# Optimization experiments

Measured on AMD Instinct MI355X. Metric: run time of the kernel, lower is better.

The kernel has to match this reference:

```python
import jax, jax.numpy as jnp
import numpy as np

N, S, HIDDEN, K, B = 20000, 16, 128, 64, 256
EPS = 0.1      # entropic blur / regularization used both in Sinkhorn and in log_pi
ITERS = 20     # fixed-point iterations (geomloss runs to tolerance; 20 converges here)


def setup_inputs() -> dict:
    key = jax.random.key(0)
    k1, k2, k3 = jax.random.split(key, 3)
    limit = float(np.sqrt(6.0 / (K + HIDDEN)))  # xavier_uniform for codebook
    return {
        "node_distributions": jax.random.normal(k1, (N, S, HIDDEN), jnp.float32),
        "batch_idx": jax.random.randint(k2, (N,), 0, B),
        "codebook": jax.random.uniform(k3, (K, HIDDEN), jnp.float32, -limit, limit),
        "log_codebook_prior": jnp.zeros((K,), jnp.float32),
        "num_graphs": B,
    }


def _sq_cost(x, y):
    # x [N,S,d], y [K,d] -> [N,S,K] squared euclidean = cdist(p=2)**2
    x2 = jnp.sum(x * x, axis=-1)[:, :, None]
    y2 = jnp.sum(y * y, axis=-1)[None, None, :]
    xy = jnp.einsum('nsd,kd->nsk', x, y)
    return jnp.maximum(x2 + y2 - 2.0 * xy, 0.0)


def _pool(node_distributions, codebook, log_codebook_prior, batch_idx, num_graphs):
    n, s, d = node_distributions.shape
    k = codebook.shape[0]
    prior = jax.nn.softmax(log_codebook_prior)     # [K]
    log_a = -jnp.log(jnp.float32(s))               # uniform node weights 1/S (scalar)
    log_b = jnp.log(prior)                         # [K]
    C = _sq_cost(node_distributions, codebook)     # [N,S,K]
    C_sg = jax.lax.stop_gradient(C)
    log_b_sg = jax.lax.stop_gradient(log_b)

    # batched log-domain Sinkhorn over all N nodes at once; loop is detached
    # (geomloss computes potentials in no_grad, grads flow via final extrapolation)
    def step(fg, _):
        f, g = fg
        g = -EPS * jax.nn.logsumexp((f[:, :, None] - C_sg) / EPS + log_a, axis=1)
        f = -EPS * jax.nn.logsumexp((g[:, None, :] - C_sg) / EPS + log_b_sg, axis=2)
        return (f, g), None

    (f, g), _ = jax.lax.scan(
        step, (jnp.zeros((n, s), C.dtype), jnp.zeros((n, k), C.dtype)), None, length=ITERS)

    # final differentiable extrapolation step
    g = -EPS * jax.nn.logsumexp((jax.lax.stop_gradient(f)[:, :, None] - C) / EPS + log_a, axis=1)
    f = -EPS * jax.nn.logsumexp((jax.lax.stop_gradient(g)[:, None, :] - C) / EPS + log_b, axis=2)

    # transport-plan marginal onto the codebook atoms (module's _compute_ot_histogram)
    log_pi = (f[:, :, None] + g[:, None, :] - C) / EPS + log_a + log_b[None, None, :]
    hist = jnp.exp(jax.nn.logsumexp(log_pi, axis=1))                 # [N,K]
    hist = hist / (jnp.sum(hist, axis=-1, keepdims=True) + 1e-12)

    # average histograms per graph; empty graphs fall back to the prior
    sums = jax.ops.segment_sum(hist, batch_idx, num_segments=num_graphs)      # [B,K]
    counts = jax.ops.segment_sum(jnp.ones((n,), hist.dtype), batch_idx,
                                 num_segments=num_graphs)                      # [B]
    return jnp.where(counts[:, None] > 0,
                     sums / jnp.maximum(counts, 1.0)[:, None],
                     prior[None, :])


def reference(node_distributions, batch_idx, codebook, log_codebook_prior, num_graphs):
    return _pool(node_distributions, codebook, log_codebook_prior, batch_idx, num_graphs)
```

## Files before the change

### kernel.cpp

```cpp
#include <hip/hip_runtime.h>
#include <math.h>

#define EPS_F 0.1f
#define L2E   1.44269504088896340736f
#define SCALE (L2E / EPS_F)
constexpr int S = 16, H = 128, K = 64, B = 256, ITERS = 20;
#define INV_S 0.0625f

template <int CTRL>
__device__ __forceinline__ float dpp_mov(float x, float old) {
  return __int_as_float(__builtin_amdgcn_update_dpp(
      __float_as_int(old), __float_as_int(x), CTRL, 0xF, 0xF, false));
}
__device__ __forceinline__ float wave_sum63(float x) {
  x += dpp_mov<0x111>(x, 0.f);
  x += dpp_mov<0x112>(x, 0.f);
  x += dpp_mov<0x114>(x, 0.f);
  x += dpp_mov<0x118>(x, 0.f);
  x += dpp_mov<0x142>(x, 0.f);
  x += dpp_mov<0x143>(x, 0.f);
  return x;
}
__device__ __forceinline__ float rl63(float x) {
  return __int_as_float(__builtin_amdgcn_readlane(__float_as_int(x), 63));
}
__device__ __forceinline__ float rfl(float x) {
  return __int_as_float(__builtin_amdgcn_readfirstlane(__float_as_int(x)));
}
#if __has_builtin(__builtin_amdgcn_exp2f)
__device__ __forceinline__ float ex2(float x) { return __builtin_amdgcn_exp2f(x); }
#else
__device__ __forceinline__ float ex2(float x) { return exp2f(x); }
#endif
#if __has_builtin(__builtin_amdgcn_logf)
__device__ __forceinline__ float lg2(float x) { return __builtin_amdgcn_logf(x); }
#else
__device__ __forceinline__ float lg2(float x) { return log2f(x); }
#endif
#if __has_builtin(__builtin_amdgcn_rcpf)
__device__ __forceinline__ float rcpa(float x) { return __builtin_amdgcn_rcpf(x); }
#else
__device__ __forceinline__ float rcpa(float x) { return 1.0f / x; }
#endif

__global__ void prep_kernel(const float* __restrict__ cb, const float* __restrict__ lp,
                            float* __restrict__ Z, float* __restrict__ y2s,
                            float* __restrict__ B2, float* __restrict__ prior) {
  const int t = threadIdx.x;
  for (int i = t; i < K * H / 4; i += 256) {
    const int c = i >> 6;
    const int k = i & 63;
    const float* p = cb + k * H + c * 4;
    float4 v;
    v.x = p[0] * (2.f * SCALE);
    v.y = p[1] * (2.f * SCALE);
    v.z = p[2] * (2.f * SCALE);
    v.w = p[3] * (2.f * SCALE);
    reinterpret_cast<float4*>(Z)[i] = v;
  }
  if (t < K) {
    const int k = t;
    float acc = 0.f;
    for (int d = 0; d < H; ++d) { const float v = cb[k * H + d]; acc = fmaf(v, v, acc); }
    y2s[k] = acc * SCALE;
    float m = -__builtin_inff();
    for (int j = 0; j < K; ++j) m = fmaxf(m, lp[j]);
    float s2 = 0.f;
    for (int j = 0; j < K; ++j) s2 += ex2((lp[j] - m) * L2E);
    const float b2 = (lp[k] - m) * L2E - lg2(s2);
    B2[k] = b2;
    prior[k] = ex2(b2);
  }
}

__global__ __launch_bounds__(256, 4)
void pool_kernel(const float* __restrict__ nd, const int* __restrict__ bidx,
                 const float* __restrict__ Z, const float* __restrict__ y2s,
                 const float* __restrict__ B2g,
                 float* __restrict__ sums, float* __restrict__ counts, int N) {
  __shared__ __align__(16) float smem[4][2064];
  const int w = threadIdx.x >> 6;
  const int lane = threadIdx.x & 63;
  const int node = blockIdx.x * 4 + w;
  if (node >= N) return;
  float* const sm = smem[w];

  const float* xp = nd + (size_t)node * (S * H);
  for (int c = 0; c < 8; ++c) {
    const int off = c * 256 + lane * 4;
    const float4 v = *reinterpret_cast<const float4*>(xp + off);
    *reinterpret_cast<float4*>(&sm[off]) = v;
    float p = v.x * v.x + v.y * v.y + v.z * v.z + v.w * v.w;
    p += __shfl_xor(p, 1);
    p += __shfl_xor(p, 2);
    p += __shfl_xor(p, 4);
    p += __shfl_xor(p, 8);
    p += __shfl_xor(p, 16);
    if ((lane & 31) == 0) sm[2048 + c * 2 + (lane >> 5)] = p;
  }

  float W[S];
  {
    const float y2k = y2s[lane];
#pragma unroll
    for (int s = 0; s < S; ++s) W[s] = -y2k;
    const float4* Z4 = reinterpret_cast<const float4*>(Z);
    for (int c = 0; c < 32; ++c) {
      const float4 z = Z4[c * 64 + lane];
#pragma unroll
      for (int s = 0; s < S; ++s) {
        const float4 x4 = *reinterpret_cast<const float4*>(&sm[s * H + c * 4]);
        W[s] = fmaf(x4.x, z.x, W[s]);
        W[s] = fmaf(x4.y, z.y, W[s]);
        W[s] = fmaf(x4.z, z.z, W[s]);
        W[s] = fmaf(x4.w, z.w, W[s]);
      }
    }
  }

  float F0[S];
  {
    const float mu = sm[2048];
#pragma unroll
    for (int s = 0; s < S; ++s) F0[s] = rfl(-(sm[2048 + s] - mu) * SCALE);
  }

  const float B2 = B2g[lane];
  const float bk = ex2(B2);
  const int ts = lane >> 2, tq = lane & 3;
  float* const trow = sm + ts * 68 + tq * 16;

  float Gt1;
  {
    float m = -__builtin_inff();
#pragma unroll
    for (int s = 0; s < S; ++s) m = fmaxf(m, F0[s] + W[s]);
    float sum = 0.f;
#pragma unroll
    for (int s = 0; s < S; ++s) sum += ex2(F0[s] + W[s] - m);
    Gt1 = -(m + lg2(sum)) + B2;
  }

#pragma unroll
  for (int s = 0; s < S; ++s) sm[s * 68 + lane] = W[s] + Gt1;
  {
    const float4 a0 = *reinterpret_cast<const float4*>(trow + 0);
    const float4 a1 = *reinterpret_cast<const float4*>(trow + 4);
    const float4 a2 = *reinterpret_cast<const float4*>(trow + 8);
    const float4 a3 = *reinterpret_cast<const float4*>(trow + 12);
    const float NI = -__builtin_inff();
    float m = fmaxf(fmaxf(fmaxf(a0.x, a0.y), fmaxf(a0.z, a0.w)),
                    fmaxf(fmaxf(a1.x, a1.y), fmaxf(a1.z, a1.w)));
    m = fmaxf(m, fmaxf(fmaxf(fmaxf(a2.x, a2.y), fmaxf(a2.z, a2.w)),
                       fmaxf(fmaxf(a3.x, a3.y), fmaxf(a3.z, a3.w))));
    m = fmaxf(m, dpp_mov<0xB1>(m, NI));
    m = fmaxf(m, dpp_mov<0x4E>(m, NI));
    float e0 = ex2(a0.x - m) + ex2(a0.y - m) + ex2(a0.z - m) + ex2(a0.w - m);
    float e1 = ex2(a1.x - m) + ex2(a1.y - m) + ex2(a1.z - m) + ex2(a1.w - m);
    float e2 = ex2(a2.x - m) + ex2(a2.y - m) + ex2(a2.z - m) + ex2(a2.w - m);
    float e3 = ex2(a3.x - m) + ex2(a3.y - m) + ex2(a3.z - m) + ex2(a3.w - m);
    float sv = (e0 + e1) + (e2 + e3);
    sv += dpp_mov<0xB1>(sv, 0.f);
    sv += dpp_mov<0x4E>(sv, 0.f);
    const float F1 = -(m + lg2(sv));
    if (tq == 0) sm[1168 + ts] = F1;
  }

  float A1K[S];
  {
    const float4 f0 = *reinterpret_cast<const float4*>(sm + 1168);
    const float4 f1 = *reinterpret_cast<const float4*>(sm + 1172);
    const float4 f2 = *reinterpret_cast<const float4*>(sm + 1176);
    const float4 f3 = *reinterpret_cast<const float4*>(sm + 1180);
    float fw[S];
    fw[0]  = f0.x + W[0];  fw[1]  = f0.y + W[1];  fw[2]  = f0.z + W[2];  fw[3]  = f0.w + W[3];
    fw[4]  = f1.x + W[4];  fw[5]  = f1.y + W[5];  fw[6]  = f1.z + W[6];  fw[7]  = f1.w + W[7];
    fw[8]  = f2.x + W[8];  fw[9]  = f2.y + W[9];  fw[10] = f2.z + W[10]; fw[11] = f2.w + W[11];
    fw[12] = f3.x + W[12]; fw[13] = f3.y + W[13]; fw[14] = f3.z + W[14]; fw[15] = f3.w + W[15];
    float m = -__builtin_inff();
#pragma unroll
    for (int s = 0; s < S; ++s) m = fmaxf(m, fw[s]);
    float sum = 0.f;
#pragma unroll
    for (int s = 0; s < S; ++s) sum += ex2(fw[s] - m);
    const float Gt2 = -(m + lg2(sum)) + B2;
#pragma unroll
    for (int s = 0; s < S; ++s) A1K[s] = ex2(fw[s] + Gt2);
  }

#pragma unroll
  for (int s = 0; s < S; ++s) sm[s * 68 + lane] = A1K[s];
  const float4 t0 = *reinterpret_cast<const float4*>(trow + 0);
  const float4 t1 = *reinterpret_cast<const float4*>(trow + 4);
  const float4 t2 = *reinterpret_cast<const float4*>(trow + 8);
  const float4 t3 = *reinterpret_cast<const float4*>(trow + 12);

  float u_prev = INV_S;
  bool active;
  {
    float r0 = ((t0.x + t0.y) + (t0.z + t0.w)) + ((t1.x + t1.y) + (t1.z + t1.w));
    float r1 = ((t2.x + t2.y) + (t2.z + t2.w)) + ((t3.x + t3.y) + (t3.z + t3.w));
    float rs = r0 + r1;
    rs += dpp_mov<0xB1>(rs, 0.f);
    rs += dpp_mov<0x4E>(rs, 0.f);
    const float u = INV_S * rcpa(fmaxf(rs, 1e-30f));
    if (tq == 0) sm[1152 + ts] = u;
    active = __any(fabsf(u - u_prev) > 6.9e-7f * u) != 0;
    u_prev = u;
  }

  if (active) for (int it = 3; it <= ITERS; ++it) {
    const float4 u0 = *reinterpret_cast<const float4*>(sm + 1152);
    const float4 u1 = *reinterpret_cast<const float4*>(sm + 1156);
    const float4 u2 = *reinterpret_cast<const float4*>(sm + 1160);
    const float4 u3 = *reinterpret_cast<const float4*>(sm + 1164);
    float p0 = A1K[0] * u0.x; p0 = fmaf(A1K[4], u1.x, p0); p0 = fmaf(A1K[8],  u2.x, p0); p0 = fmaf(A1K[12], u3.x, p0);
    float p1 = A1K[1] * u0.y; p1 = fmaf(A1K[5], u1.y, p1); p1 = fmaf(A1K[9],  u2.y, p1); p1 = fmaf(A1K[13], u3.y, p1);
    float p2 = A1K[2] * u0.z; p2 = fmaf(A1K[6], u1.z, p2); p2 = fmaf(A1K[10], u2.z, p2); p2 = fmaf(A1K[14], u3.z, p2);
    float p3 = A1K[3] * u0.w; p3 = fmaf(A1K[7], u1.w, p3); p3 = fmaf(A1K[11], u2.w, p3); p3 = fmaf(A1K[15], u3.w, p3);
    const float cs = (p0 + p1) + (p2 + p3);
    sm[1088 + lane] = bk * rcpa(fmaxf(cs, 1e-30f));

    const float* vrow = sm + 1088 + tq * 16;
    const float4 v0 = *reinterpret_cast<const float4*>(vrow + 0);
    const float4 v1 = *reinterpret_cast<const float4*>(vrow + 4);
    const float4 v2 = *reinterpret_cast<const float4*>(vrow + 8);
    const float4 v3 = *reinterpret_cast<const float4*>(vrow + 12);
    float r0 = t0.x * v0.x; r0 = fmaf(t1.x, v1.x, r0); r0 = fmaf(t2.x, v2.x, r0); r0 = fmaf(t3.x, v3.x, r0);
    float r1 = t0.y * v0.y; r1 = fmaf(t1.y, v1.y, r1); r1 = fmaf(t2.y, v2.y, r1); r1 = fmaf(t3.y, v3.y, r1);
    float r2 = t0.z * v0.z; r2 = fmaf(t1.z, v1.z, r2); r2 = fmaf(t2.z, v2.z, r2); r2 = fmaf(t3.z, v3.z, r2);
    float r3 = t0.w * v0.w; r3 = fmaf(t1.w, v1.w, r3); r3 = fmaf(t2.w, v2.w, r3); r3 = fmaf(t3.w, v3.w, r3);
    float rs = (r0 + r1) + (r2 + r3);
    rs += dpp_mov<0xB1>(rs, 0.f);
    rs += dpp_mov<0x4E>(rs, 0.f);
    const float u = INV_S * rcpa(fmaxf(rs, 1e-30f));
    if (tq == 0) sm[1152 + ts] = u;
    const bool moved = fabsf(u - u_prev) > 6.9e-7f * u;
    u_prev = u;
    if (!__any(moved)) break;
  }


  float Fc[S];
  {
    const float4 f0 = *reinterpret_cast<const float4*>(sm + 1168);
    const float4 f1 = *reinterpret_cast<const float4*>(sm + 1172);
    const float4 f2 = *reinterpret_cast<const float4*>(sm + 1176);
    const float4 f3 = *reinterpret_cast<const float4*>(sm + 1180);
    const float4 u0 = *reinterpret_cast<const float4*>(sm + 1152);
    const float4 u1 = *reinterpret_cast<const float4*>(sm + 1156);
    const float4 u2 = *reinterpret_cast<const float4*>(sm + 1160);
    const float4 u3 = *reinterpret_cast<const float4*>(sm + 1164);
    Fc[0]  = f0.x + lg2(16.f * u0.x); Fc[1]  = f0.y + lg2(16.f * u0.y);
    Fc[2]  = f0.z + lg2(16.f * u0.z); Fc[3]  = f0.w + lg2(16.f * u0.w);
    Fc[4]  = f1.x + lg2(16.f * u1.x); Fc[5]  = f1.y + lg2(16.f * u1.y);
    Fc[6]  = f1.z + lg2(16.f * u1.z); Fc[7]  = f1.w + lg2(16.f * u1.w);
    Fc[8]  = f2.x + lg2(16.f * u2.x); Fc[9]  = f2.y + lg2(16.f * u2.y);
    Fc[10] = f2.z + lg2(16.f * u2.z); Fc[11] = f2.w + lg2(16.f * u2.w);
    Fc[12] = f3.x + lg2(16.f * u3.x); Fc[13] = f3.y + lg2(16.f * u3.y);
    Fc[14] = f3.z + lg2(16.f * u3.z); Fc[15] = f3.w + lg2(16.f * u3.w);
  }

  float Gt;
  {
    float m = -__builtin_inff();
#pragma unroll
    for (int s = 0; s < S; ++s) m = fmaxf(m, Fc[s] + W[s]);
    float sum = 0.f;
#pragma unroll
    for (int s = 0; s < S; ++s) sum += ex2(Fc[s] + W[s] - m);
    Gt = -(m + lg2(sum)) + B2;
  }

#pragma unroll
  for (int s = 0; s < S; ++s) sm[s * 68 + lane] = W[s] + Gt;
  {
    const float4 a0 = *reinterpret_cast<const float4*>(trow + 0);
    const float4 a1 = *reinterpret_cast<const float4*>(trow + 4);
    const float4 a2 = *reinterpret_cast<const float4*>(trow + 8);
    const float4 a3 = *reinterpret_cast<const float4*>(trow + 12);
    const float NI = -__builtin_inff();
    float m = fmaxf(fmaxf(fmaxf(a0.x, a0.y), fmaxf(a0.z, a0.w)),
                    fmaxf(fmaxf(a1.x, a1.y), fmaxf(a1.z, a1.w)));
    m = fmaxf(m, fmaxf(fmaxf(fmaxf(a2.x, a2.y), fmaxf(a2.z, a2.w)),
                       fmaxf(fmaxf(a3.x, a3.y), fmaxf(a3.z, a3.w))));
    m = fmaxf(m, dpp_mov<0xB1>(m, NI));
    m = fmaxf(m, dpp_mov<0x4E>(m, NI));
    float e0 = ex2(a0.x - m) + ex2(a0.y - m) + ex2(a0.z - m) + ex2(a0.w - m);
    float e1 = ex2(a1.x - m) + ex2(a1.y - m) + ex2(a1.z - m) + ex2(a1.w - m);
    float e2 = ex2(a2.x - m) + ex2(a2.y - m) + ex2(a2.z - m) + ex2(a2.w - m);
    float e3 = ex2(a3.x - m) + ex2(a3.y - m) + ex2(a3.z - m) + ex2(a3.w - m);
    float sv = (e0 + e1) + (e2 + e3);
    sv += dpp_mov<0xB1>(sv, 0.f);
    sv += dpp_mov<0x4E>(sv, 0.f);
    const float F21 = -(m + lg2(sv));
    if (tq == 0) sm[1168 + ts] = F21;
  }

  {
    const float4 f0 = *reinterpret_cast<const float4*>(sm + 1168);
    const float4 f1 = *reinterpret_cast<const float4*>(sm + 1172);
    const float4 f2 = *reinterpret_cast<const float4*>(sm + 1176);
    const float4 f3 = *reinterpret_cast<const float4*>(sm + 1180);
    float Ff[S];
    Ff[0]  = f0.x; Ff[1]  = f0.y; Ff[2]  = f0.z; Ff[3]  = f0.w;
    Ff[4]  = f1.x; Ff[5]  = f1.y; Ff[6]  = f1.z; Ff[7]  = f1.w;
    Ff[8]  = f2.x; Ff[9]  = f2.y; Ff[10] = f2.z; Ff[11] = f2.w;
    Ff[12] = f3.x; Ff[13] = f3.y; Ff[14] = f3.z; Ff[15] = f3.w;
    float h = 0.f;
#pragma unroll
    for (int s = 0; s < S; ++s) h += ex2(Ff[s] + Gt + W[s]);
    const float tot = rl63(wave_sum63(h));
    const float hn = h / (tot + 1e-12f);
    const int b = bidx[node];
    atomicAdd(&sums[b * K + lane], hn);
    if (lane == 0) atomicAdd(&counts[b], 1.f);
  }
}

__global__ void finish_kernel(const float* __restrict__ sums, const float* __restrict__ counts,
                              const float* __restrict__ prior, float* __restrict__ out) {
  const int t = blockIdx.x * 256 + threadIdx.x;
  if (t >= B * K) return;
  const int b = t >> 6;
  const int k = t & 63;
  const float c = counts[b];
  out[t] = (c > 0.f) ? sums[t] / fmaxf(c, 1.f) : prior[k];
}

extern "C" void kernel_launch(void* const* d_in, const int* in_sizes, int n_in,
                              void* d_out, int out_size, void* d_ws, size_t ws_size,
                              hipStream_t stream) {
  const float* nd  = (const float*)d_in[0];
  const int*   bx  = (const int*)d_in[1];
  const float* cb  = (const float*)d_in[2];
  const float* lp  = (const float*)d_in[3];
  const int N = in_sizes[1];

  float* ws     = (float*)d_ws;
  float* sums   = ws;
  float* counts = ws + B * K;
  float* Z      = counts + B;
  float* y2s    = Z + K * H;
  float* B2     = y2s + K;
  float* prior  = B2 + K;

  hipMemsetAsync(ws, 0, (size_t)(B * K + B) * sizeof(float), stream);
  prep_kernel<<<1, 256, 0, stream>>>(cb, lp, Z, y2s, B2, prior);
  pool_kernel<<<(N + 3) / 4, 256, 0, stream>>>(nd, bx, Z, y2s, B2, sums, counts, N);
  finish_kernel<<<(B * K + 255) / 256, 256, 0, stream>>>(sums, counts, prior, (float*)d_out);
}
```

Measured before the change: 367.2 us.

## Halve per-wave LDS staging, use packed FMA, and raise occupancy bound

Result: slower. 379.1 us (+3.2%).

```diff
diff --git a/kernel.cpp b/kernel.cpp
--- a/kernel.cpp
+++ b/kernel.cpp
@@ -6,6 +6,8 @@
 #define SCALE (L2E / EPS_F)
 constexpr int S = 16, H = 128, K = 64, B = 256, ITERS = 20;
 #define INV_S 0.0625f
+
+typedef float vf2 __attribute__((ext_vector_type(2)));
 
 template <int CTRL>
 __device__ __forceinline__ float dpp_mov(float x, float old) {
@@ -42,6 +44,13 @@
 #else
 __device__ __forceinline__ float rcpa(float x) { return 1.0f / x; }
 #endif
+__device__ __forceinline__ vf2 pkfma(vf2 a, vf2 b, vf2 c) {
+#if __has_builtin(__builtin_elementwise_fma)
+  return __builtin_elementwise_fma(a, b, c);
+#else
+  vf2 r; r.x = fmaf(a.x, b.x, c.x); r.y = fmaf(a.y, b.y, c.y); return r;
+#endif
+}
 
 __global__ void prep_kernel(const float* __restrict__ cb, const float* __restrict__ lp,
                             float* __restrict__ Z, float* __restrict__ y2s,
@@ -73,12 +82,12 @@
   }
 }
 
-__global__ __launch_bounds__(256, 4)
+__global__ __launch_bounds__(256, 8)
 void pool_kernel(const float* __restrict__ nd, const int* __restrict__ bidx,
                  const float* __restrict__ Z, const float* __restrict__ y2s,
                  const float* __restrict__ B2g,
                  float* __restrict__ sums, float* __restrict__ counts, int N) {
-  __shared__ __align__(16) float smem[4][2064];
+  __shared__ __align__(16) float smem[4][1200];
   const int w = threadIdx.x >> 6;
   const int lane = threadIdx.x & 63;
   const int node = blockIdx.x * 4 + w;
@@ -86,43 +95,49 @@
   float* const sm = smem[w];
 
   const float* xp = nd + (size_t)node * (S * H);
-  for (int c = 0; c < 8; ++c) {
-    const int off = c * 256 + lane * 4;
-    const float4 v = *reinterpret_cast<const float4*>(xp + off);
-    *reinterpret_cast<float4*>(&sm[off]) = v;
-    float p = v.x * v.x + v.y * v.y + v.z * v.z + v.w * v.w;
-    p += __shfl_xor(p, 1);
-    p += __shfl_xor(p, 2);
-    p += __shfl_xor(p, 4);
-    p += __shfl_xor(p, 8);
-    p += __shfl_xor(p, 16);
-    if ((lane & 31) == 0) sm[2048 + c * 2 + (lane >> 5)] = p;
-  }
-
-  float W[S];
-  {
-    const float y2k = y2s[lane];
-#pragma unroll
-    for (int s = 0; s < S; ++s) W[s] = -y2k;
-    const float4* Z4 = reinterpret_cast<const float4*>(Z);
+  const float4* Z4 = reinterpret_cast<const float4*>(Z);
+  const float y2k = y2s[lane];
+  vf2 W2[S];
+#pragma unroll
+  for (int s = 0; s < S; ++s) { W2[s].x = -y2k; W2[s].y = 0.f; }
+#pragma unroll
+  for (int p = 0; p < 2; ++p) {
+#pragma unroll
+    for (int c8 = 0; c8 < 4; ++c8) {
+      const int off = c8 * 256 + lane * 4;
+      const float4 v = *reinterpret_cast<const float4*>(xp + p * 1024 + off);
+      *reinterpret_cast<float4*>(&sm[off]) = v;
+      float pp = v.x * v.x + v.y * v.y + v.z * v.z + v.w * v.w;
+      pp += __shfl_xor(pp, 1);
+      pp += __shfl_xor(pp, 2);
+      pp += __shfl_xor(pp, 4);
+      pp += __shfl_xor(pp, 8);
+      pp += __shfl_xor(pp, 16);
+      if ((lane & 31) == 0) sm[1184 + p * 8 + c8 * 2 + (lane >> 5)] = pp;
+    }
     for (int c = 0; c < 32; ++c) {
       const float4 z = Z4[c * 64 + lane];
-#pragma unroll
-      for (int s = 0; s < S; ++s) {
-        const float4 x4 = *reinterpret_cast<const float4*>(&sm[s * H + c * 4]);
-        W[s] = fmaf(x4.x, z.x, W[s]);
-        W[s] = fmaf(x4.y, z.y, W[s]);
-        W[s] = fmaf(x4.z, z.z, W[s]);
-        W[s] = fmaf(x4.w, z.w, W[s]);
+      vf2 zlo; zlo.x = z.x; zlo.y = z.y;
+      vf2 zhi; zhi.x = z.z; zhi.y = z.w;
+#pragma unroll
+      for (int sl = 0; sl < 8; ++sl) {
+        const float4 x4 = *reinterpret_cast<const float4*>(&sm[sl * 128 + c * 4]);
+        vf2 xlo; xlo.x = x4.x; xlo.y = x4.y;
+        vf2 xhi; xhi.x = x4.z; xhi.y = x4.w;
+        W2[p * 8 + sl] = pkfma(xlo, zlo, W2[p * 8 + sl]);
+        W2[p * 8 + sl] = pkfma(xhi, zhi, W2[p * 8 + sl]);
       }
     }
   }
+  float W[S];
+#pragma unroll
+  for (int s = 0; s < S; ++s) W[s] = W2[s].x + W2[s].y;
 
   float F0[S];
   {
-    const float mu = sm[2048];
-#pragma unroll
-    for (int s = 0; s < S; ++s) F0[s] = rfl(-(sm[2048 + s] - mu) * SCALE);
+    const float mu = sm[1184];
+#pragma unroll
+    for (int s = 0; s < S; ++s) F0[s] = rfl(-(sm[1184 + s] - mu) * SCALE);
   }
 
   const float B2 = B2g[lane];
```
